# Optimization experiments

Hardware: AMD Instinct MI355X
Metric: run time of the kernel (lower is better)

## Reference

```python
import math
import jax, jax.numpy as jnp
import numpy as np

D_MODEL = 1024
D_FF = 4096
NUM_EXPERTS = 8
CAPACITY_FACTOR = 1.0
ALPHA = 0.01
Z_LOSS_COEF = 0.001


def setup_inputs() -> dict:
    key = jax.random.key(0)
    kx, kr, k1, k2, kb1, kb2 = jax.random.split(key, 6)
    init_scale = 0.1
    x = jax.random.normal(kx, (8, 2048, D_MODEL), dtype=jnp.float32)
    # torch Linear weight [out,in] with truncated-normal std=init_scale*sqrt(1/fan_in);
    # stored here in math layout: y = x @ W
    w_router = jax.random.normal(kr, (D_MODEL, NUM_EXPERTS), jnp.float32) * (init_scale * math.sqrt(1.0 / D_MODEL))
    w1 = jax.random.normal(k1, (NUM_EXPERTS, D_MODEL, D_FF), jnp.float32) * (init_scale * math.sqrt(1.0 / D_MODEL))
    w2 = jax.random.normal(k2, (NUM_EXPERTS, D_FF, D_MODEL), jnp.float32) * (init_scale * math.sqrt(1.0 / D_FF))
    b1 = jnp.zeros((NUM_EXPERTS, D_FF), jnp.float32)
    b2 = jnp.zeros((NUM_EXPERTS, D_MODEL), jnp.float32)
    return {"x": x, "w_router": w_router, "w1": w1, "b1": b1, "w2": w2, "b2": b2}


def reference(x, w_router, w1, b1, w2, b2):
    # Eval-mode forward (no router noise, no dropout), as in is_training=False.
    d = x.shape[-1]
    E = w1.shape[0]
    tokens = x.reshape(-1, d)                       # [T, d]
    T = tokens.shape[0]

    router_logits = tokens @ w_router               # [T, E]
    router_probs = jax.nn.softmax(router_logits.astype(jnp.float32), axis=-1)
    top1_prob = jnp.max(router_probs, axis=-1)      # [T]
    top1_idx = jnp.argmax(router_probs, axis=-1)    # [T]

    # load-balancing aux loss
    counts = jnp.zeros((E,), jnp.float32).at[top1_idx].add(1.0)
    fi = jax.lax.stop_gradient(counts / T)
    Pi = router_probs.mean(axis=0)
    aux_loss = ALPHA * E * jnp.dot(fi, Pi)
    z_loss = jnp.mean(jnp.square(jax.scipy.special.logsumexp(router_logits, axis=-1)))
    aux_loss = aux_loss + Z_LOSS_COEF * z_loss

    # capacity-limited first-come-first-serve positions per expert
    C = max(int(math.ceil(T / float(E) * CAPACITY_FACTOR)), 1)
    onehot = (top1_idx[:, None] == jnp.arange(E)[None, :]).astype(jnp.int32)  # [T, E]
    cum = jnp.cumsum(onehot, axis=0)
    pos = jnp.take_along_axis(cum, top1_idx[:, None], axis=1)[:, 0] - 1       # [T]
    fits = pos < C                                                            # [T]
    pos_c = jnp.clip(pos, 0, C - 1)

    # dispatch: dropped tokens contribute zeros (collision-safe add)
    contrib = tokens * fits[:, None].astype(tokens.dtype)
    expert_inputs = jnp.zeros((E, C, d), tokens.dtype).at[top1_idx, pos_c].add(contrib)

    # per-expert FFN as batched GEMMs
    h = jax.nn.relu(jnp.einsum('ecd,edf->ecf', expert_inputs, w1) + b1[:, None, :])
    expert_outputs = jnp.einsum('ecf,efd->ecd', h, w2) + b2[:, None, :]       # [E, C, d]

    # combine: fitted tokens get prob-weighted expert output, dropped tokens pass through
    gathered = expert_outputs[top1_idx, pos_c]                                # [T, d]
    scaled = gathered * top1_prob[:, None].astype(gathered.dtype)
    outputs_tokens = jnp.where(fits[:, None], scaled, tokens)
    return outputs_tokens.reshape(x.shape), aux_loss
```

## Files before the change

### kernel.cpp

```cpp
#include <hip/hip_runtime.h>
#include <stdint.h>
#include <stddef.h>

typedef __attribute__((ext_vector_type(4))) float floatx4;
typedef __attribute__((ext_vector_type(8))) int intx8;

#define T_TOK 16384
#define DM 1024
#define DF 4096
#define NE 8
#define CAP 2048

#define SCALE_ONE 127
#define SCALE_W   121

static __device__ __forceinline__ int pk4(float a, float b, float c, float d) {
  int v = __builtin_amdgcn_cvt_pk_fp8_f32(a, b, 0, false);
  v = __builtin_amdgcn_cvt_pk_fp8_f32(c, d, v, true);
  return v;
}

static __device__ __forceinline__ void async_cp16(const void* g, void* l) {
  typedef const unsigned int __attribute__((address_space(1)))* gp_t;
  typedef unsigned int __attribute__((address_space(3)))* lp_t;
  __builtin_amdgcn_global_load_lds((gp_t)g, (lp_t)l, 16, 0, 0);
}

__global__ void init_kernel(int* __restrict__ src_token) {
  int i = blockIdx.x * 256 + threadIdx.x;
  if (i < NE * CAP) src_token[i] = -1;
}

__global__ void __launch_bounds__(256, 4) router_kernel(
    const float* __restrict__ x, const float* __restrict__ wr,
    int* __restrict__ top_idx, float* __restrict__ top_prob,
    float* __restrict__ part) {
  __shared__ float wl[8][1024];
  __shared__ float bstat[4][12];
  int tid = threadIdx.x;
  int lane = tid & 63, w = tid >> 6;

#pragma unroll
  for (int r = 0; r < 8; r++) {
    int j = tid + 256 * r;
    float4 v = ((const float4*)wr)[j];
    int f = j >> 1;
    int e0 = (j & 1) * 4;
    wl[e0 + 0][f] = v.x;
    wl[e0 + 1][f] = v.y;
    wl[e0 + 2][f] = v.z;
    wl[e0 + 3][f] = v.w;
  }
  __syncthreads();

  int t0 = blockIdx.x * 8 + w * 2;

  float4 xa[2][4];
#pragma unroll
  for (int tok = 0; tok < 2; tok++)
#pragma unroll
    for (int i = 0; i < 4; i++)
      xa[tok][i] = *(const float4*)&x[(size_t)(t0 + tok) * DM + i * 256 + lane * 4];

  float acc[2][8];
#pragma unroll
  for (int tok = 0; tok < 2; tok++)
#pragma unroll
    for (int e = 0; e < 8; e++) acc[tok][e] = 0.f;

#pragma unroll
  for (int i = 0; i < 4; i++) {
    float4 wv[8];
#pragma unroll
    for (int e = 0; e < 8; e++)
      wv[e] = *(const float4*)&wl[e][i * 256 + lane * 4];
#pragma unroll
    for (int tok = 0; tok < 2; tok++) {
      float4 xv = xa[tok][i];
#pragma unroll
      for (int e = 0; e < 8; e++)
        acc[tok][e] = fmaf(xv.x, wv[e].x,
                      fmaf(xv.y, wv[e].y,
                      fmaf(xv.z, wv[e].z,
                      fmaf(xv.w, wv[e].w, acc[tok][e]))));
    }
  }

  float pi_acc[8] = {0, 0, 0, 0, 0, 0, 0, 0};
  float z_acc = 0.f;
#pragma unroll
  for (int tok = 0; tok < 2; tok++) {
    float a[8];
#pragma unroll
    for (int e = 0; e < 8; e++) a[e] = acc[tok][e];
#pragma unroll
    for (int off = 32; off > 0; off >>= 1)
#pragma unroll
      for (int e = 0; e < 8; e++) a[e] += __shfl_xor(a[e], off, 64);
    float mx = a[0]; int mi = 0;
#pragma unroll
    for (int e = 1; e < 8; e++) { if (a[e] > mx) { mx = a[e]; mi = e; } }
    float s = 0.f, pr[8];
#pragma unroll
    for (int e = 0; e < 8; e++) { pr[e] = __expf(a[e] - mx); s += pr[e]; }
    float inv = 1.f / s;
#pragma unroll
    for (int e = 0; e < 8; e++) pi_acc[e] += pr[e] * inv;
    float lse = mx + __logf(s);
    z_acc += lse * lse;
    if (lane == 0) { top_idx[t0 + tok] = mi; top_prob[t0 + tok] = pr[mi] * inv; }
  }

  if (lane == 0) {
#pragma unroll
    for (int e = 0; e < 8; e++) bstat[w][e] = pi_acc[e];
    bstat[w][8] = z_acc;
  }
  __syncthreads();
  if (tid < 9) {
    float s = bstat[0][tid] + bstat[1][tid] + bstat[2][tid] + bstat[3][tid];
    part[(size_t)blockIdx.x * 16 + tid] = s;
  }
}

__global__ void __launch_bounds__(1024) scan_kernel(
    const int* __restrict__ top_idx, const float* __restrict__ part,
    int* __restrict__ dest_slot, int* __restrict__ src_token,
    float* __restrict__ aux_out) {
  __shared__ int cnt[1024 * 9];
  __shared__ float sstat[16][12];
  int tid = threadIdx.x;

  float ps[9];
#pragma unroll
  for (int e = 0; e < 9; e++) ps[e] = 0.f;
#pragma unroll
  for (int rr = 0; rr < 2; rr++) {
    const float* pp = &part[(size_t)(tid + rr * 1024) * 16];
#pragma unroll
    for (int e = 0; e < 9; e++) ps[e] += pp[e];
  }
#pragma unroll
  for (int off = 32; off > 0; off >>= 1)
#pragma unroll
    for (int e = 0; e < 9; e++) ps[e] += __shfl_xor(ps[e], off, 64);
  if ((tid & 63) == 0) {
#pragma unroll
    for (int e = 0; e < 9; e++) sstat[tid >> 6][e] = ps[e];
  }

  int eloc[16];
  int c[8] = {0, 0, 0, 0, 0, 0, 0, 0};
#pragma unroll
  for (int i = 0; i < 16; i++) {
    int e = top_idx[tid * 16 + i];
    eloc[i] = e;
    c[e]++;
  }
#pragma unroll
  for (int e = 0; e < 8; e++) cnt[tid * 9 + e] = c[e];
  __syncthreads();
  for (int s = 1; s < 1024; s <<= 1) {
    int v[8];
    if (tid >= s) {
#pragma unroll
      for (int e = 0; e < 8; e++) v[e] = cnt[(tid - s) * 9 + e];
    }
    __syncthreads();
    if (tid >= s) {
#pragma unroll
      for (int e = 0; e < 8; e++) cnt[tid * 9 + e] += v[e];
    }
    __syncthreads();
  }
  int run[8];
#pragma unroll
  for (int e = 0; e < 8; e++) run[e] = cnt[tid * 9 + e] - c[e];
#pragma unroll
  for (int i = 0; i < 16; i++) {
    int t = tid * 16 + i;
    int e = eloc[i];
    int pos = run[e]++;
    int d = (pos < CAP) ? (e * CAP + pos) : -1;
    dest_slot[t] = d;
    if (d >= 0) src_token[d] = t;
  }
  if (tid == 1023) {
    float st[9];
#pragma unroll
    for (int e = 0; e < 9; e++) {
      float s = 0.f;
      for (int ww = 0; ww < 16; ww++) s += sstat[ww][e];
      st[e] = s;
    }
    float aux = 0.f;
    for (int e = 0; e < 8; e++)
      aux += ((float)cnt[1023 * 9 + e] / (float)T_TOK) * (st[e] / (float)T_TOK);
    aux = 0.01f * 8.f * aux + 0.001f * (st[8] / (float)T_TOK);
    *aux_out = aux;
  }
}

__global__ void __launch_bounds__(256) dispatch_kernel(
    const float* __restrict__ x, const int* __restrict__ src_token,
    unsigned char* __restrict__ A) {
  int slot = blockIdx.x;
  int tid = threadIdx.x;
  int src = src_token[slot];
  int v = 0;
  if (src >= 0) {
    float4 xv = *(const float4*)&x[(size_t)src * DM + tid * 4];
    v = pk4(xv.x, xv.y, xv.z, xv.w);
  }
  *(int*)&A[(size_t)slot * DM + tid * 4] = v;
}

__global__ void __launch_bounds__(256) transpose_cast_kernel(
    const float* __restrict__ src, unsigned char* __restrict__ dst,
    int K, int N) {
  __shared__ float tile[64][65];
  int e = blockIdx.z;
  int n0 = blockIdx.x * 64, k0 = blockIdx.y * 64;
  int tid = threadIdx.x;
  int tx = tid & 63, ty = tid >> 6;
  const float* S = src + (size_t)e * K * N;
  unsigned char* D = dst + (size_t)e * N * K;
#pragma unroll
  for (int r = 0; r < 16; r++) {
    int k = ty + r * 4;
    tile[k][tx] = S[(size_t)(k0 + k) * N + n0 + tx];
  }
  __syncthreads();
  int n = tid >> 2, kq = (tid & 3) * 16;
  int4 ov;
  int w[4];
#pragma unroll
  for (int g = 0; g < 4; g++) {
    int kk = kq + g * 4;
    w[g] = pk4(tile[kk + 0][n] * 64.f, tile[kk + 1][n] * 64.f,
               tile[kk + 2][n] * 64.f, tile[kk + 3][n] * 64.f);
  }
  ov.x = w[0]; ov.y = w[1]; ov.z = w[2]; ov.w = w[3];
  *(int4*)&D[(size_t)(n0 + n) * K + k0 + kq] = ov;
}


__global__ void __launch_bounds__(512, 2) gemm1_kernel(
    const unsigned char* __restrict__ A, const unsigned char* __restrict__ BT,
    const float* __restrict__ b1, unsigned char* __restrict__ H) {
  __shared__ __align__(16) unsigned char As[256 * 128];
  __shared__ __align__(16) unsigned char Bs[256 * 128];
  int e = blockIdx.z;
  int plane = blockIdx.x + 16 * blockIdx.y;
  int nid = (plane & 7) * 16 + (plane >> 3);
  int n0 = (nid & 15) * 256, m0 = (nid >> 4) * 256;
  const unsigned char* Ae = A + ((size_t)e * CAP + m0) * DM;
  const unsigned char* Be = BT + ((size_t)e * DF + n0) * DM;
  int tid = threadIdx.x;
  int lane = tid & 63, wid = tid >> 6;
  int wmi = wid >> 2, wni = wid & 3;
  int l15 = lane & 15, q = lane >> 4;
  floatx4 acc[8][4];
#pragma unroll
  for (int i = 0; i < 8; i++)
#pragma unroll
    for (int j = 0; j < 4; j++) acc[i][j] = (floatx4){0.f, 0.f, 0.f, 0.f};

  for (int kb = 0; kb < DM; kb += 128) {
#pragma unroll
    for (int r = 0; r < 4; r++) {
      int c = tid + 512 * r;
      int row = c >> 3, cc = c & 7;
      int ccs = cc ^ (row & 7);
      async_cp16(Ae + (size_t)row * DM + kb + ccs * 16, As + c * 16);
      async_cp16(Be + (size_t)row * DM + kb + ccs * 16, Bs + c * 16);
    }
    __syncthreads();
#pragma unroll
    for (int ph = 0; ph < 4; ph++) {
      const int Mh = ph >> 1, Nh = ph & 1;
      intx8 af[4], bf[2];
#pragma unroll
      for (int i = 0; i < 4; i++) {
        int row = wmi * 128 + (Mh * 4 + i) * 16 + l15;
        int sw = row & 7;
        int4 lo = *(const int4*)&As[row * 128 + ((2 * q) ^ sw) * 16];
        int4 hi = *(const int4*)&As[row * 128 + ((2 * q + 1) ^ sw) * 16];
        af[i] = (intx8){lo.x, lo.y, lo.z, lo.w, hi.x, hi.y, hi.z, hi.w};
      }
#pragma unroll
      for (int j = 0; j < 2; j++) {
        int row = wni * 64 + (Nh * 2 + j) * 16 + l15;
        int sw = row & 7;
        int4 lo = *(const int4*)&Bs[row * 128 + ((2 * q) ^ sw) * 16];
        int4 hi = *(const int4*)&Bs[row * 128 + ((2 * q + 1) ^ sw) * 16];
        bf[j] = (intx8){lo.x, lo.y, lo.z, lo.w, hi.x, hi.y, hi.z, hi.w};
      }
#pragma unroll
      for (int i = 0; i < 4; i++)
#pragma unroll
        for (int j = 0; j < 2; j++)
          acc[Mh * 4 + i][Nh * 2 + j] = __builtin_amdgcn_mfma_scale_f32_16x16x128_f8f6f4(
              bf[j], af[i], acc[Mh * 4 + i][Nh * 2 + j], 0, 0, 0, SCALE_W, 0, SCALE_ONE);
    }
    __syncthreads();
  }
  const float* b1e = b1 + e * DF;
#pragma unroll
  for (int i = 0; i < 8; i++) {
    int m = m0 + wmi * 128 + i * 16 + l15;
    unsigned char* hrow = H + ((size_t)e * CAP + m) * DF;
#pragma unroll
    for (int j = 0; j < 4; j++) {
      int nb = n0 + wni * 64 + j * 16 + q * 4;
      float4 bv = *(const float4*)&b1e[nb];
      floatx4 a = acc[i][j];
      *(int*)&hrow[nb] = pk4(fmaxf(a[0] + bv.x, 0.f), fmaxf(a[1] + bv.y, 0.f),
                             fmaxf(a[2] + bv.z, 0.f), fmaxf(a[3] + bv.w, 0.f));
    }
  }
}

__global__ void __launch_bounds__(512, 2) gemm2_kernel(
    const unsigned char* __restrict__ Hm, const unsigned char* __restrict__ BT,
    const float* __restrict__ b2, const int* __restrict__ src_token,
    const float* __restrict__ top_prob, float* __restrict__ out) {
  __shared__ __align__(16) unsigned char As[256 * 128];
  __shared__ __align__(16) unsigned char Bs[256 * 128];
  int e = blockIdx.z;
  int plane = blockIdx.x + 4 * blockIdx.y;
  int nid = (plane & 7) * 4 + (plane >> 3);
  int n0 = (nid & 3) * 256, m0 = (nid >> 2) * 256;
  const unsigned char* Ae = Hm + ((size_t)e * CAP + m0) * DF;
  const unsigned char* Be = BT + ((size_t)e * DM + n0) * DF;
  int tid = threadIdx.x;
  int lane = tid & 63, wid = tid >> 6;
  int wmi = wid >> 2, wni = wid & 3;
  int l15 = lane & 15, q = lane >> 4;
  floatx4 acc[8][4];
#pragma unroll
  for (int i = 0; i < 8; i++)
#pragma unroll
    for (int j = 0; j < 4; j++) acc[i][j] = (floatx4){0.f, 0.f, 0.f, 0.f};

  for (int kb = 0; kb < DF; kb += 128) {
#pragma unroll
    for (int r = 0; r < 4; r++) {
      int c = tid + 512 * r;
      int row = c >> 3, cc = c & 7;
      int ccs = cc ^ (row & 7);
      async_cp16(Ae + (size_t)row * DF + kb + ccs * 16, As + c * 16);
      async_cp16(Be + (size_t)row * DF + kb + ccs * 16, Bs + c * 16);
    }
    __syncthreads();
#pragma unroll
    for (int ph = 0; ph < 4; ph++) {
      const int Mh = ph >> 1, Nh = ph & 1;
      intx8 af[4], bf[2];
#pragma unroll
      for (int i = 0; i < 4; i++) {
        int row = wmi * 128 + (Mh * 4 + i) * 16 + l15;
        int sw = row & 7;
        int4 lo = *(const int4*)&As[row * 128 + ((2 * q) ^ sw) * 16];
        int4 hi = *(const int4*)&As[row * 128 + ((2 * q + 1) ^ sw) * 16];
        af[i] = (intx8){lo.x, lo.y, lo.z, lo.w, hi.x, hi.y, hi.z, hi.w};
      }
#pragma unroll
      for (int j = 0; j < 2; j++) {
        int row = wni * 64 + (Nh * 2 + j) * 16 + l15;
        int sw = row & 7;
        int4 lo = *(const int4*)&Bs[row * 128 + ((2 * q) ^ sw) * 16];
        int4 hi = *(const int4*)&Bs[row * 128 + ((2 * q + 1) ^ sw) * 16];
        bf[j] = (intx8){lo.x, lo.y, lo.z, lo.w, hi.x, hi.y, hi.z, hi.w};
      }
#pragma unroll
      for (int i = 0; i < 4; i++)
#pragma unroll
        for (int j = 0; j < 2; j++)
          acc[Mh * 4 + i][Nh * 2 + j] = __builtin_amdgcn_mfma_scale_f32_16x16x128_f8f6f4(
              bf[j], af[i], acc[Mh * 4 + i][Nh * 2 + j], 0, 0, 0, SCALE_W, 0, SCALE_ONE);
    }
    __syncthreads();
  }
  const float* b2e = b2 + e * DM;
#pragma unroll
  for (int i = 0; i < 8; i++) {
    int m = m0 + wmi * 128 + i * 16 + l15;
    int t = src_token[e * CAP + m];
    if (t < 0) continue;
    float p = top_prob[t];
    float* orow = out + (size_t)t * DM;
#pragma unroll
    for (int j = 0; j < 4; j++) {
      int nb = n0 + wni * 64 + j * 16 + q * 4;
      float4 bv = *(const float4*)&b2e[nb];
      floatx4 a = acc[i][j];
      float4 o;
      o.x = p * (a[0] + bv.x);
      o.y = p * (a[1] + bv.y);
      o.z = p * (a[2] + bv.z);
      o.w = p * (a[3] + bv.w);
      *(float4*)&orow[nb] = o;
    }
  }
}

__global__ void __launch_bounds__(256) passthru_kernel(
    const float* __restrict__ x, const int* __restrict__ dest_slot,
    float* __restrict__ out) {
  int t = blockIdx.x;
  if (dest_slot[t] >= 0) return;
  int c = threadIdx.x * 4;
  *(float4*)&out[(size_t)t * DM + c] = *(const float4*)&x[(size_t)t * DM + c];
}

extern "C" void kernel_launch(void* const* d_in, const int* in_sizes, int n_in,
                              void* d_out, int out_size, void* d_ws, size_t ws_size,
                              hipStream_t stream) {
  const float* x  = (const float*)d_in[0];
  const float* wr = (const float*)d_in[1];
  const float* w1 = (const float*)d_in[2];
  const float* b1 = (const float*)d_in[3];
  const float* w2 = (const float*)d_in[4];
  const float* b2 = (const float*)d_in[5];
  float* out = (float*)d_out;

  const size_t OFF_A    = 0;
  const size_t OFF_W1T  = 16777216;
  const size_t OFF_W2T  = 50331648;
  const size_t OFF_H    = 83886080;
  const size_t OFF_TIDX = 150994944;
  const size_t OFF_TPRB = 151060480;
  const size_t OFF_DEST = 151126016;
  const size_t OFF_SRC  = 151191552;
  const size_t OFF_STAT = 151257088;
  if (ws_size < OFF_STAT + 64) return;

  char* ws = (char*)d_ws;
  unsigned char* A_f8 = (unsigned char*)(ws + OFF_A);
  float* part = (float*)(ws + OFF_A);
  unsigned char* W1T  = (unsigned char*)(ws + OFF_W1T);
  unsigned char* W2T  = (unsigned char*)(ws + OFF_W2T);
  unsigned char* Hbuf = (unsigned char*)(ws + OFF_H);
  int*   top_idx   = (int*)(ws + OFF_TIDX);
  float* top_prob  = (float*)(ws + OFF_TPRB);
  int*   dest_slot = (int*)(ws + OFF_DEST);
  int*   src_token = (int*)(ws + OFF_SRC);

  hipLaunchKernelGGL(init_kernel, dim3(64), dim3(256), 0, stream, src_token);
  hipLaunchKernelGGL(router_kernel, dim3(2048), dim3(256), 0, stream,
                     x, wr, top_idx, top_prob, part);
  hipLaunchKernelGGL(scan_kernel, dim3(1), dim3(1024), 0, stream,
                     top_idx, part, dest_slot, src_token, out + (size_t)T_TOK * DM);
  hipLaunchKernelGGL(dispatch_kernel, dim3(NE * CAP), dim3(256), 0, stream,
                     x, src_token, A_f8);
  hipLaunchKernelGGL(transpose_cast_kernel, dim3(DF / 64, DM / 64, NE), dim3(256), 0, stream,
                     w1, W1T, DM, DF);
  hipLaunchKernelGGL(transpose_cast_kernel, dim3(DM / 64, DF / 64, NE), dim3(256), 0, stream,
                     w2, W2T, DF, DM);
  hipLaunchKernelGGL(gemm1_kernel, dim3(DF / 256, CAP / 256, NE), dim3(512), 0, stream,
                     A_f8, W1T, b1, Hbuf);
  hipLaunchKernelGGL(gemm2_kernel, dim3(DM / 256, CAP / 256, NE), dim3(512), 0, stream,
                     Hbuf, W2T, b2, src_token, top_prob, out);
  hipLaunchKernelGGL(passthru_kernel, dim3(T_TOK), dim3(256), 0, stream,
                     x, dest_slot, out);
}
```

Baseline: 626.3 us.

## Double-buffer LDS tiles in both expert GEMMs to prefetch the next K-slice

Both FP8 expert GEMM kernels now hold two LDS buffers each for the A and B tiles. The next 128-wide K-slice is loaded asynchronously while MFMAs run on the current slice, and an explicit vmcnt drain plus barrier ends each iteration. The goal is to hide global-to-LDS load latency inside each block. The cost is doubled LDS per block, 128KB instead of 64KB, which likely allows only one 512-thread block per CU instead of the two the launch bounds target. That lost cross-block overlap may cancel the intra-block prefetch gain.

```diff
diff --git a/kernel.cpp b/kernel.cpp
--- a/kernel.cpp
+++ b/kernel.cpp
@@ -24,6 +24,12 @@
   typedef const unsigned int __attribute__((address_space(1)))* gp_t;
   typedef unsigned int __attribute__((address_space(3)))* lp_t;
   __builtin_amdgcn_global_load_lds((gp_t)g, (lp_t)l, 16, 0, 0);
+}
+
+static __device__ __forceinline__ void drain_and_sync() {
+  asm volatile("s_waitcnt vmcnt(0)" ::: "memory");
+  __builtin_amdgcn_sched_barrier(0);
+  __syncthreads();
 }
 
 __global__ void init_kernel(int* __restrict__ src_token) {
@@ -248,8 +254,8 @@
 __global__ void __launch_bounds__(512, 2) gemm1_kernel(
     const unsigned char* __restrict__ A, const unsigned char* __restrict__ BT,
     const float* __restrict__ b1, unsigned char* __restrict__ H) {
-  __shared__ __align__(16) unsigned char As[256 * 128];
-  __shared__ __align__(16) unsigned char Bs[256 * 128];
+  __shared__ __align__(16) unsigned char As_[2][256 * 128];
+  __shared__ __align__(16) unsigned char Bs_[2][256 * 128];
   int e = blockIdx.z;
   int plane = blockIdx.x + 16 * blockIdx.y;
   int nid = (plane & 7) * 16 + (plane >> 3);
@@ -266,16 +272,32 @@
 #pragma unroll
     for (int j = 0; j < 4; j++) acc[i][j] = (floatx4){0.f, 0.f, 0.f, 0.f};
 
-  for (int kb = 0; kb < DM; kb += 128) {
-#pragma unroll
-    for (int r = 0; r < 4; r++) {
-      int c = tid + 512 * r;
-      int row = c >> 3, cc = c & 7;
-      int ccs = cc ^ (row & 7);
-      async_cp16(Ae + (size_t)row * DM + kb + ccs * 16, As + c * 16);
-      async_cp16(Be + (size_t)row * DM + kb + ccs * 16, Bs + c * 16);
-    }
-    __syncthreads();
+  const int NT = DM / 128;
+#pragma unroll
+  for (int r = 0; r < 4; r++) {
+    int c = tid + 512 * r;
+    int row = c >> 3, cc = c & 7;
+    int ccs = cc ^ (row & 7);
+    async_cp16(Ae + (size_t)row * DM + 0 + ccs * 16, As_[0] + c * 16);
+    async_cp16(Be + (size_t)row * DM + 0 + ccs * 16, Bs_[0] + c * 16);
+  }
+  drain_and_sync();
+
+  int cur = 0;
+  for (int t = 0; t < NT; t++) {
+    if (t + 1 < NT) {
+      int kb = (t + 1) * 128;
+#pragma unroll
+      for (int r = 0; r < 4; r++) {
+        int c = tid + 512 * r;
+        int row = c >> 3, cc = c & 7;
+        int ccs = cc ^ (row & 7);
+        async_cp16(Ae + (size_t)row * DM + kb + ccs * 16, As_[cur ^ 1] + c * 16);
+        async_cp16(Be + (size_t)row * DM + kb + ccs * 16, Bs_[cur ^ 1] + c * 16);
+      }
+    }
+    const unsigned char* Asc = As_[cur];
+    const unsigned char* Bsc = Bs_[cur];
 #pragma unroll
     for (int ph = 0; ph < 4; ph++) {
       const int Mh = ph >> 1, Nh = ph & 1;
@@ -284,16 +306,16 @@
       for (int i = 0; i < 4; i++) {
         int row = wmi * 128 + (Mh * 4 + i) * 16 + l15;
         int sw = row & 7;
-        int4 lo = *(const int4*)&As[row * 128 + ((2 * q) ^ sw) * 16];
-        int4 hi = *(const int4*)&As[row * 128 + ((2 * q + 1) ^ sw) * 16];
+        int4 lo = *(const int4*)&Asc[row * 128 + ((2 * q) ^ sw) * 16];
+        int4 hi = *(const int4*)&Asc[row * 128 + ((2 * q + 1) ^ sw) * 16];
         af[i] = (intx8){lo.x, lo.y, lo.z, lo.w, hi.x, hi.y, hi.z, hi.w};
       }
 #pragma unroll
       for (int j = 0; j < 2; j++) {
         int row = wni * 64 + (Nh * 2 + j) * 16 + l15;
         int sw = row & 7;
-        int4 lo = *(const int4*)&Bs[row * 128 + ((2 * q) ^ sw) * 16];
-        int4 hi = *(const int4*)&Bs[row * 128 + ((2 * q + 1) ^ sw) * 16];
+        int4 lo = *(const int4*)&Bsc[row * 128 + ((2 * q) ^ sw) * 16];
+        int4 hi = *(const int4*)&Bsc[row * 128 + ((2 * q + 1) ^ sw) * 16];
         bf[j] = (intx8){lo.x, lo.y, lo.z, lo.w, hi.x, hi.y, hi.z, hi.w};
       }
 #pragma unroll
@@ -303,7 +325,8 @@
           acc[Mh * 4 + i][Nh * 2 + j] = __builtin_amdgcn_mfma_scale_f32_16x16x128_f8f6f4(
               bf[j], af[i], acc[Mh * 4 + i][Nh * 2 + j], 0, 0, 0, SCALE_W, 0, SCALE_ONE);
     }
-    __syncthreads();
+    drain_and_sync();
+    cur ^= 1;
   }
   const float* b1e = b1 + e * DF;
 #pragma unroll
@@ -325,8 +348,8 @@
     const unsigned char* __restrict__ Hm, const unsigned char* __restrict__ BT,
     const float* __restrict__ b2, const int* __restrict__ src_token,
     const float* __restrict__ top_prob, float* __restrict__ out) {
-  __shared__ __align__(16) unsigned char As[256 * 128];
-  __shared__ __align__(16) unsigned char Bs[256 * 128];
+  __shared__ __align__(16) unsigned char As_[2][256 * 128];
+  __shared__ __align__(16) unsigned char Bs_[2][256 * 128];
   int e = blockIdx.z;
   int plane = blockIdx.x + 4 * blockIdx.y;
   int nid = (plane & 7) * 4 + (plane >> 3);
@@ -343,16 +366,32 @@
 #pragma unroll
     for (int j = 0; j < 4; j++) acc[i][j] = (floatx4){0.f, 0.f, 0.f, 0.f};
 
-  for (int kb = 0; kb < DF; kb += 128) {
-#pragma unroll
-    for (int r = 0; r < 4; r++) {
-      int c = tid + 512 * r;
-      int row = c >> 3, cc = c & 7;
-      int ccs = cc ^ (row & 7);
-      async_cp16(Ae + (size_t)row * DF + kb + ccs * 16, As + c * 16);
-      async_cp16(Be + (size_t)row * DF + kb + ccs * 16, Bs + c * 16);
-    }
-    __syncthreads();
+  const int NT = DF / 128;
+#pragma unroll
+  for (int r = 0; r < 4; r++) {
+    int c = tid + 512 * r;
+    int row = c >> 3, cc = c & 7;
+    int ccs = cc ^ (row & 7);
+    async_cp16(Ae + (size_t)row * DF + 0 + ccs * 16, As_[0] + c * 16);
+    async_cp16(Be + (size_t)row * DF + 0 + ccs * 16, Bs_[0] + c * 16);
+  }
+  drain_and_sync();
+
+  int cur = 0;
+  for (int t = 0; t < NT; t++) {
+    if (t + 1 < NT) {
+      int kb = (t + 1) * 128;
+#pragma unroll
+      for (int r = 0; r < 4; r++) {
+        int c = tid + 512 * r;
+        int row = c >> 3, cc = c & 7;
+        int ccs = cc ^ (row & 7);
+        async_cp16(Ae + (size_t)row * DF + kb + ccs * 16, As_[cur ^ 1] + c * 16);
+        async_cp16(Be + (size_t)row * DF + kb + ccs * 16, Bs_[cur ^ 1] + c * 16);
+      }
+    }
+    const unsigned char* Asc = As_[cur];
+    const unsigned char* Bsc = Bs_[cur];
 #pragma unroll
     for (int ph = 0; ph < 4; ph++) {
       const int Mh = ph >> 1, Nh = ph & 1;
@@ -361,16 +400,16 @@
       for (int i = 0; i < 4; i++) {
         int row = wmi * 128 + (Mh * 4 + i) * 16 + l15;
         int sw = row & 7;
-        int4 lo = *(const int4*)&As[row * 128 + ((2 * q) ^ sw) * 16];
-        int4 hi = *(const int4*)&As[row * 128 + ((2 * q + 1) ^ sw) * 16];
+        int4 lo = *(const int4*)&Asc[row * 128 + ((2 * q) ^ sw) * 16];
+        int4 hi = *(const int4*)&Asc[row * 128 + ((2 * q + 1) ^ sw) * 16];
         af[i] = (intx8){lo.x, lo.y, lo.z, lo.w, hi.x, hi.y, hi.z, hi.w};
       }
 #pragma unroll
       for (int j = 0; j < 2; j++) {
         int row = wni * 64 + (Nh * 2 + j) * 16 + l15;
         int sw = row & 7;
-        int4 lo = *(const int4*)&Bs[row * 128 + ((2 * q) ^ sw) * 16];
-        int4 hi = *(const int4*)&Bs[row * 128 + ((2 * q + 1) ^ sw) * 16];
+        int4 lo = *(const int4*)&Bsc[row * 128 + ((2 * q) ^ sw) * 16];
+        int4 hi = *(const int4*)&Bsc[row * 128 + ((2 * q + 1) ^ sw) * 16];
         bf[j] = (intx8){lo.x, lo.y, lo.z, lo.w, hi.x, hi.y, hi.z, hi.w};
       }
 #pragma unroll
@@ -380,7 +419,8 @@
           acc[Mh * 4 + i][Nh * 2 + j] = __builtin_amdgcn_mfma_scale_f32_16x16x128_f8f6f4(
               bf[j], af[i], acc[Mh * 4 + i][Nh * 2 + j], 0, 0, 0, SCALE_W, 0, SCALE_ONE);
     }
-    __syncthreads();
+    drain_and_sync();
+    cur ^= 1;
   }
   const float* b2e = b2 + e * DM;
 #pragma unroll
```

Measured after the change: 615.8 us. Within noise of the previous version (-1.7%).
